# Kernel tuning notes

Hardware: AMD Instinct MI355X
Metric: run time of the kernel (lower is better)

## Reference

```python
import jax, jax.numpy as jnp
import numpy as np

FEATS = 768
HEAD = 12
HD = FEATS // HEAD


def setup_inputs() -> dict:
    key = jax.random.key(0)
    ks = jax.random.split(key, 10)
    b, n, f = 8, 1024, FEATS
    s = 1.0 / np.sqrt(f)
    return {
        "x": jax.random.normal(ks[0], (b, n, f), dtype=jnp.float32),
        "bias": jnp.zeros((), dtype=jnp.float32),
        "Wq": jax.random.normal(ks[1], (f, f), dtype=jnp.float32) * s,
        "bq": jnp.zeros((f,), dtype=jnp.float32),
        "Wk": jax.random.normal(ks[2], (f, f), dtype=jnp.float32) * s,
        "bk": jnp.zeros((f,), dtype=jnp.float32),
        "Wv": jax.random.normal(ks[3], (f, f), dtype=jnp.float32) * s,
        "bv": jnp.zeros((f,), dtype=jnp.float32),
        "Wo": jax.random.normal(ks[4], (f, f), dtype=jnp.float32) * s,
        "bo": jnp.zeros((f,), dtype=jnp.float32),
    }


def reference(x, bias, Wq, bq, Wk, bk, Wv, bv, Wo, bo):
    b, n, f = x.shape
    sqrt_d = jnp.sqrt(jnp.asarray(f, dtype=x.dtype))  # scale uses full feats, per source

    def split_heads(t):  # (b,n,f) -> (b,h,n,hd)
        return t.reshape(b, n, HEAD, HD).transpose(0, 2, 1, 3)

    q = split_heads(x @ Wq.T + bq)
    k = split_heads(x @ Wk.T + bk)
    v = split_heads(x @ Wv.T + bv)

    # sigmoid attention: no row-wise normalization
    score = jax.nn.sigmoid(jnp.einsum('bhif,bhjf->bhij', q, k) / sqrt_d + bias)
    attn = jnp.einsum('bhij,bhjf->bihf', score, v)  # (b,n,h,hd)
    o = attn.reshape(b, n, f) @ Wo.T + bo  # dropout p=0.0 -> identity
    return o
```

## Files before the change

### kernel.cpp

```cpp
#include <hip/hip_runtime.h>

#define FEATS 768
#define NHEAD 12
#define HD    64
#define SEQ   1024
#define NB    8
#define MROWS (NB*SEQ)
#define NQK   (2*FEATS)
#define QKVN  (3*FEATS)
#define QSC   0.0520616136f

typedef __attribute__((ext_vector_type(8))) __bf16          bf16x8;
typedef __attribute__((ext_vector_type(4))) __bf16          bf16x4;
typedef __attribute__((ext_vector_type(4))) unsigned short  us4;
typedef __attribute__((ext_vector_type(4))) float           f32x4;

__device__ __forceinline__ unsigned short f2bf(float f) {
  union { float f; unsigned u; } v; v.f = f;
  return (unsigned short)((v.u + 0x7fffu + ((v.u >> 16) & 1u)) >> 16);
}

__device__ __forceinline__ void gload_lds16(const void* g, void* l) {
  __builtin_amdgcn_global_load_lds(
      (const __attribute__((address_space(1))) void*)g,
      (__attribute__((address_space(3))) void*)l, 16, 0, 0);
}

__global__ void cast_all(const float* __restrict__ x,
                         const float* __restrict__ Wq, const float* __restrict__ Wk,
                         const float* __restrict__ Wv, const float* __restrict__ Wo,
                         const float* __restrict__ bq, const float* __restrict__ bk,
                         const float* __restrict__ bv,
                         unsigned short* __restrict__ Xbf,
                         unsigned short* __restrict__ Wcat,
                         unsigned short* __restrict__ Wobf,
                         float* __restrict__ bcat) {
  int blk = blockIdx.x;
  if (blk < 6144) {
    int i = blk * 256 + threadIdx.x;
    f32x4 v = ((const f32x4*)x)[i];
    us4 o;
    o[0] = f2bf(v[0]); o[1] = f2bf(v[1]); o[2] = f2bf(v[2]); o[3] = f2bf(v[3]);
    ((us4*)Xbf)[i] = o;
  } else if (blk < 8448) {
    int bb = blk - 6144;
    int mtx = bb / 576;
    int i = (bb % 576) * 256 + threadIdx.x;
    const float* src = (mtx == 0) ? Wq : (mtx == 1) ? Wk : (mtx == 2) ? Wv : Wo;
    f32x4 v = ((const f32x4*)src)[i];
    us4 o;
    o[0] = f2bf(v[0]); o[1] = f2bf(v[1]); o[2] = f2bf(v[2]); o[3] = f2bf(v[3]);
    if (mtx < 3) ((us4*)Wcat)[mtx * 147456 + i] = o;
    else         ((us4*)Wobf)[i] = o;
  } else {
    int i = (blk - 8448) * 256 + threadIdx.x;
    if (i < QKVN)
      bcat[i] = (i < FEATS) ? bq[i] : (i < 2*FEATS ? bk[i-FEATS] : bv[i-2*FEATS]);
  }
}

#define FOFF(row) ((row)*64 + (((g) ^ (((row) >> 1) & 3)) << 4))

__global__ __launch_bounds__(256, 3) void gemm1_bt(
    const unsigned short* __restrict__ A,
    const unsigned short* __restrict__ B,
    const float* __restrict__ bias,
    unsigned short* __restrict__ QKo,
    unsigned short* __restrict__ VTo)
{
  __shared__ __align__(16) char Al[2 * 8192];
  __shared__ __align__(16) char Bl[2 * 12288];

  const int tid  = threadIdx.x;
  const int lane = tid & 63;
  const int w    = tid >> 6;
  const int l15  = lane & 15;
  const int g    = lane >> 4;
  const int wm   = (w >> 1) * 64;
  const int wn   = (w & 1) * 96;

  const int id  = blockIdx.x;
  const int xcd = id & 7;
  const int j   = id >> 3;
  const int mi  = xcd * 8 + (j & 7);
  const int ni  = j >> 3;
  const int mbase = mi * 128;
  const int nbase = ni * 192;

  const int trow  = tid >> 2;
  const int sslot = ((tid & 3) ^ ((tid >> 3) & 3)) * 8;
  const unsigned short* Ag = A + (size_t)(mbase + trow) * 768 + sslot;
  const unsigned short* Bg = B + (size_t)(nbase + trow) * 768 + sslot;

  auto STAGE = [&](int buf, int t) {
    const unsigned short* sa = Ag + t * 32;
    const unsigned short* sb = Bg + t * 32;
    char* da = Al + buf * 8192  + tid * 16;
    char* db = Bl + buf * 12288 + tid * 16;
    gload_lds16(sa,            da);
    gload_lds16(sa + 64*768,   da + 4096);
    gload_lds16(sb,            db);
    gload_lds16(sb + 64*768,   db + 4096);
    gload_lds16(sb + 128*768,  db + 8192);
  };

  f32x4 acc[4][6] = {};

  STAGE(0, 0);
  asm volatile("s_waitcnt vmcnt(0)" ::: "memory");
  __builtin_amdgcn_s_barrier();

  for (int t = 0; t < 24; t++) {
    if (t < 23) STAGE((t + 1) & 1, t + 1);

    const char* Ab = Al + (t & 1) * 8192;
    const char* Bb = Bl + (t & 1) * 12288;
    bf16x8 af[4];
#pragma unroll
    for (int mf = 0; mf < 4; mf++) {
      const int row = wm + mf*16 + l15;
      af[mf] = *(const bf16x8*)(Ab + FOFF(row));
    }
    __builtin_amdgcn_s_setprio(1);
#pragma unroll
    for (int nf = 0; nf < 6; nf++) {
      const int row = wn + nf*16 + l15;
      bf16x8 bfv = *(const bf16x8*)(Bb + FOFF(row));
#pragma unroll
      for (int mf = 0; mf < 4; mf++)
        acc[mf][nf] = __builtin_amdgcn_mfma_f32_16x16x32_bf16(af[mf], bfv, acc[mf][nf], 0, 0, 0);
    }
    __builtin_amdgcn_s_setprio(0);

    if (t < 23) {
      asm volatile("s_waitcnt vmcnt(0)" ::: "memory");
      __builtin_amdgcn_s_barrier();
    }
  }

  const bool isQK = (ni < 8);
  const float osc = (ni < 4) ? QSC : 1.0f;
#pragma unroll
  for (int mf = 0; mf < 4; mf++)
#pragma unroll
    for (int nf = 0; nf < 6; nf++) {
      const int col  = nbase + wn + nf*16 + l15;
      const float bb = bias[col];
      const int row0 = mbase + wm + mf*16 + g*4;
      if (isQK) {
#pragma unroll
        for (int r = 0; r < 4; r++)
          QKo[(size_t)(row0 + r)*NQK + col] = f2bf((acc[mf][nf][r] + bb) * osc);
      } else {
        const int c  = col - NQK;
        const int hh = c >> 6, dd = c & 63;
        const int bI = row0 >> 10, n0 = row0 & 1023;
        us4 o;
#pragma unroll
        for (int r = 0; r < 4; r++) o[r] = f2bf(acc[mf][nf][r] + bb);
        *(us4*)(VTo + ((size_t)((bI*NHEAD + hh)*HD + dd))*SEQ + n0) = o;
      }
    }
}

__global__ __launch_bounds__(256, 4) void gemm2_bt(
    const unsigned short* __restrict__ A,
    const unsigned short* __restrict__ B,
    const float* __restrict__ bias,
    float* __restrict__ C)
{
  __shared__ __align__(16) char Al[2 * 4096];
  __shared__ __align__(16) char Bl[2 * 8192];

  const int tid  = threadIdx.x;
  const int lane = tid & 63;
  const int w    = tid >> 6;
  const int l15  = lane & 15;
  const int g    = lane >> 4;
  const int wm   = (w >> 1) * 32;
  const int wn   = (w & 1) * 64;

  const int id  = blockIdx.x;
  const int xcd = id & 7;
  const int j   = id >> 3;
  const int mi  = xcd * 16 + (j & 15);
  const int ni  = j >> 4;
  const int mbase = mi * 64;
  const int nbase = ni * 128;

  const int trow  = tid >> 2;
  const int sslot = ((tid & 3) ^ ((tid >> 3) & 3)) * 8;
  const unsigned short* Ag = A + (size_t)(mbase + trow) * 768 + sslot;
  const unsigned short* Bg = B + (size_t)(nbase + trow) * 768 + sslot;

  auto STAGE = [&](int buf, int t) {
    const unsigned short* sa = Ag + t * 32;
    const unsigned short* sb = Bg + t * 32;
    char* da = Al + buf * 4096 + tid * 16;
    char* db = Bl + buf * 8192 + tid * 16;
    gload_lds16(sa,           da);
    gload_lds16(sb,           db);
    gload_lds16(sb + 64*768,  db + 4096);
  };

  f32x4 acc[2][4] = {};

  STAGE(0, 0);
  asm volatile("s_waitcnt vmcnt(0)" ::: "memory");
  __builtin_amdgcn_s_barrier();

  for (int t = 0; t < 24; t++) {
    if (t < 23) STAGE((t + 1) & 1, t + 1);

    const char* Ab = Al + (t & 1) * 4096;
    const char* Bb = Bl + (t & 1) * 8192;
    bf16x8 af[2], bfv[4];
#pragma unroll
    for (int mf = 0; mf < 2; mf++) {
      const int row = wm + mf*16 + l15;
      af[mf] = *(const bf16x8*)(Ab + FOFF(row));
    }
#pragma unroll
    for (int nf = 0; nf < 4; nf++) {
      const int row = wn + nf*16 + l15;
      bfv[nf] = *(const bf16x8*)(Bb + FOFF(row));
    }
    __builtin_amdgcn_s_setprio(1);
#pragma unroll
    for (int mf = 0; mf < 2; mf++)
#pragma unroll
      for (int nf = 0; nf < 4; nf++)
        acc[mf][nf] = __builtin_amdgcn_mfma_f32_16x16x32_bf16(af[mf], bfv[nf], acc[mf][nf], 0, 0, 0);
    __builtin_amdgcn_s_setprio(0);

    if (t < 23) {
      asm volatile("s_waitcnt vmcnt(0)" ::: "memory");
      __builtin_amdgcn_s_barrier();
    }
  }

#pragma unroll
  for (int mf = 0; mf < 2; mf++)
#pragma unroll
    for (int nf = 0; nf < 4; nf++) {
      const int col  = nbase + wn + nf*16 + l15;
      const float bb = bias[col];
      const int row0 = mbase + wm + mf*16 + g*4;
#pragma unroll
      for (int r = 0; r < 4; r++)
        C[(size_t)(row0 + r)*FEATS + col] = acc[mf][nf][r] + bb;
    }
}
#undef FOFF

__global__ __launch_bounds__(256, 3) void attn_kernel(
    const unsigned short* __restrict__ QK,
    const unsigned short* __restrict__ VT,
    const float* __restrict__ biasp,
    unsigned short* __restrict__ AO)
{
  __shared__ __align__(16) char Kl[2][8192];
  __shared__ __align__(16) char Vl[2][8192];
  __shared__ __align__(16) char Sl[4][4096];

  const int tid  = threadIdx.x;
  const int lane = tid & 63;
  const int w    = tid >> 6;
  const int l15  = lane & 15;
  const int g    = lane >> 4;

  const int id  = blockIdx.x;
  const int r8  = id & 7;
  const int m   = id >> 3;
  const int bh  = r8 * 12 + (m >> 3);
  const int qx  = m & 7;
  const int b   = bh / NHEAD;
  const int h   = bh % NHEAD;
  const int rowB  = b * SEQ;
  const int qbase = rowB + qx * 128;

  const float Kb = __builtin_amdgcn_exp2f(-biasp[0] * 1.4426950408889634f);

  bf16x8 qf[2][2];
  {
    const unsigned short* qp = QK + (size_t)(qbase + w*32 + l15) * NQK + h*HD + g*8;
    qf[0][0] = *(const bf16x8*)(qp);
    qf[0][1] = *(const bf16x8*)(qp + 32);
    qf[1][0] = *(const bf16x8*)(qp + 16*NQK);
    qf[1][1] = *(const bf16x8*)(qp + 16*NQK + 32);
  }

  const int trow = tid >> 3;
  const int colb = ((tid & 7) * 16) ^ ((trow & 7) << 4);
  const char* Ksrc = (const char*)QK +
      ((size_t)(rowB + trow) * NQK + FEATS + h*HD) * 2 + colb;
  const char* Vsrc = (const char*)VT +
      ((size_t)(bh*HD + trow)) * (SEQ*2) + colb;

  auto STAGE_K = [&](int p, int t) {
    char* kw = Kl[p] + tid*16;
    gload_lds16(Ksrc + (size_t)t * 64 * (NQK*2),              kw);
    gload_lds16(Ksrc + (size_t)t * 64 * (NQK*2) + 32*(NQK*2), kw + 4096);
  };
  auto STAGE_V = [&](int p, int t) {
    char* vw = Vl[p] + tid*16;
    gload_lds16(Vsrc + t * 128,              vw);
    gload_lds16(Vsrc + t * 128 + 32*(SEQ*2), vw + 4096);
  };

  char* Sw = Sl[w];
  f32x4 o_acc[4][2] = {};
  f32x4 sE[2][4], sO[2][4];

  auto SIGPV = [&](f32x4 (&sP)[2][4], const char* Vp) {
#pragma unroll
    for (int qm = 0; qm < 2; qm++)
#pragma unroll
      for (int nf = 0; nf < 4; nf++) {
        bf16x4 pk;
#pragma unroll
        for (int rr = 0; rr < 4; rr++) {
          const float e = __builtin_amdgcn_exp2f(-sP[qm][nf][rr]);
          pk[rr] = (__bf16)__builtin_amdgcn_rcpf(__builtin_fmaf(Kb, e, 1.0f));
        }
        const int sq = qm*16 + l15;
        const int by = (sq*128 + (nf*16 + g*4)*2) ^ ((sq & 7) << 4);
        *(bf16x4*)(Sw + by) = pk;
      }
#pragma unroll
    for (int js = 0; js < 2; js++) {
      bf16x8 sf[2];
#pragma unroll
      for (int qm = 0; qm < 2; qm++) {
        const int sq = qm*16 + l15;
        const int by = (sq*128 + js*64 + g*16) ^ ((sq & 7) << 4);
        sf[qm] = *(const bf16x8*)(Sw + by);
      }
      bf16x8 vf[4];
#pragma unroll
      for (int df = 0; df < 4; df++) {
        const int row = df*16 + l15;
        const int by  = (row*128 + js*64 + g*16) ^ ((row & 7) << 4);
        vf[df] = *(const bf16x8*)(Vp + by);
      }
      __builtin_amdgcn_s_setprio(1);
#pragma unroll
      for (int df = 0; df < 4; df++)
#pragma unroll
        for (int qm = 0; qm < 2; qm++)
          o_acc[df][qm] = __builtin_amdgcn_mfma_f32_16x16x32_bf16(vf[df], sf[qm], o_acc[df][qm], 0, 0, 0);
      __builtin_amdgcn_s_setprio(0);
    }
  };

  auto BODY = [&](int t, f32x4 (&sC)[2][4], f32x4 (&sP)[2][4], bool stK, bool doPrev) {
    if (stK) STAGE_K((t + 1) & 1, t + 1);
    STAGE_V(t & 1, t);

    const char* Kp = Kl[t & 1];
#pragma unroll
    for (int qm = 0; qm < 2; qm++)
#pragma unroll
      for (int nf = 0; nf < 4; nf++)
        sC[qm][nf] = (f32x4){0.f, 0.f, 0.f, 0.f};
    __builtin_amdgcn_s_setprio(1);
#pragma unroll
    for (int nf = 0; nf < 4; nf++)
#pragma unroll
      for (int ks = 0; ks < 2; ks++) {
        const int row = nf*16 + l15;
        const int by  = (row*128 + ks*64 + g*16) ^ ((row & 7) << 4);
        bf16x8 kf = *(const bf16x8*)(Kp + by);
        sC[0][nf] = __builtin_amdgcn_mfma_f32_16x16x32_bf16(kf, qf[0][ks], sC[0][nf], 0, 0, 0);
        sC[1][nf] = __builtin_amdgcn_mfma_f32_16x16x32_bf16(kf, qf[1][ks], sC[1][nf], 0, 0, 0);
      }
    __builtin_amdgcn_s_setprio(0);

    if (doPrev) SIGPV(sP, Vl[(t - 1) & 1]);

    __syncthreads();
  };

  STAGE_K(0, 0);
  __syncthreads();

  BODY(0, sE, sO, true, false);
#pragma unroll 1
  for (int t = 1; t < 15; t += 2) {
    BODY(t,     sO, sE, true, true);
    BODY(t + 1, sE, sO, true, true);
  }
  BODY(15, sO, sE, false, true);
  SIGPV(sO, Vl[1]);

  unsigned short* aop = AO + (size_t)(qbase + w*32) * FEATS + h*HD;
#pragma unroll
  for (int df = 0; df < 4; df++)
#pragma unroll
    for (int qm = 0; qm < 2; qm++) {
      const int q  = qm*16 + l15;
      const int d0 = df*16 + g*4;
      bf16x4 o;
#pragma unroll
      for (int rr = 0; rr < 4; rr++) o[rr] = (__bf16)o_acc[df][qm][rr];
      *(bf16x4*)(aop + (size_t)q * FEATS + d0) = o;
    }
}

extern "C" void kernel_launch(void* const* d_in, const int* in_sizes, int n_in,
                              void* d_out, int out_size, void* d_ws, size_t ws_size,
                              hipStream_t stream) {
  const float* x    = (const float*)d_in[0];
  const float* bias = (const float*)d_in[1];
  const float* Wq   = (const float*)d_in[2];
  const float* bq   = (const float*)d_in[3];
  const float* Wk   = (const float*)d_in[4];
  const float* bk   = (const float*)d_in[5];
  const float* Wv   = (const float*)d_in[6];
  const float* bv   = (const float*)d_in[7];
  const float* Wo   = (const float*)d_in[8];
  const float* bo   = (const float*)d_in[9];
  float* out = (float*)d_out;

  char* ws = (char*)d_ws;
  unsigned short* Xbf  = (unsigned short*)(ws + 0);
  unsigned short* Wcat = (unsigned short*)(ws + 12582912);
  unsigned short* Wobf = (unsigned short*)(ws + 16121856);
  float*          bcat = (float*)        (ws + 17301504);
  unsigned short* QKb  = (unsigned short*)(ws + 17310720);
  unsigned short* VTb  = (unsigned short*)(ws + 42476544);
  unsigned short* AO   = Xbf;

  cast_all<<<8457, 256, 0, stream>>>(x, Wq, Wk, Wv, Wo, bq, bk, bv,
                                     Xbf, Wcat, Wobf, bcat);

  gemm1_bt<<<768, 256, 0, stream>>>(Xbf, Wcat, bcat, QKb, VTb);

  attn_kernel<<<768, 256, 0, stream>>>(QKb, VTb, bias, AO);

  gemm2_bt<<<768, 256, 0, stream>>>(AO, Wobf, bo, out);
}
```

Before: 108.1 us.

## Keep sigmoid scores in registers by permuting V^T key order

The QKV GEMM epilogue now writes V^T with a permuted key order inside each 64-key block, so the sigmoid scores produced by the QK^T MFMA can be fed directly as the B operand of the PV MFMA from registers. This removes the per-wave LDS scratch buffer and its write/read round trip, along with the associated LDS traffic and latency. LDS use per block drops, which may allow more resident blocks. The change relies on the producer and consumer agreeing exactly on the permutation.

```diff
diff --git a/kernel.cpp b/kernel.cpp
--- a/kernel.cpp
+++ b/kernel.cpp
@@ -155,10 +155,13 @@
         const int c  = col - NQK;
         const int hh = c >> 6, dd = c & 63;
         const int bI = row0 >> 10, n0 = row0 & 1023;
+        const int rl  = n0 & 63;
+        const int cp  = ((rl >> 5) << 5) | (((rl >> 2) & 3) << 3) | (((rl >> 4) & 1) << 2);
+        const int n0p = (n0 & ~63) | cp;
         us4 o;
 #pragma unroll
         for (int r = 0; r < 4; r++) o[r] = f2bf(acc[mf][nf][r] + bb);
-        *(us4*)(VTo + ((size_t)((bI*NHEAD + hh)*HD + dd))*SEQ + n0) = o;
+        *(us4*)(VTo + ((size_t)((bI*NHEAD + hh)*HD + dd))*SEQ + n0p) = o;
       }
     }
 }
@@ -261,7 +264,6 @@
 {
   __shared__ __align__(16) char Kl[2][8192];
   __shared__ __align__(16) char Vl[2][8192];
-  __shared__ __align__(16) char Sl[4][4096];
 
   const int tid  = threadIdx.x;
   const int lane = tid & 63;
@@ -308,34 +310,34 @@
     gload_lds16(Vsrc + t * 128 + 32*(SEQ*2), vw + 4096);
   };
 
-  char* Sw = Sl[w];
   f32x4 o_acc[4][2] = {};
   f32x4 sE[2][4], sO[2][4];
 
   auto SIGPV = [&](f32x4 (&sP)[2][4], const char* Vp) {
-#pragma unroll
-    for (int qm = 0; qm < 2; qm++)
-#pragma unroll
-      for (int nf = 0; nf < 4; nf++) {
-        bf16x4 pk;
+    bf16x8 paq[2][2];
+#pragma unroll
+    for (int qm = 0; qm < 2; qm++) {
+      float sg[4][4];
+#pragma unroll
+      for (int nf = 0; nf < 4; nf++)
 #pragma unroll
         for (int rr = 0; rr < 4; rr++) {
           const float e = __builtin_amdgcn_exp2f(-sP[qm][nf][rr]);
-          pk[rr] = (__bf16)__builtin_amdgcn_rcpf(__builtin_fmaf(Kb, e, 1.0f));
+          sg[nf][rr] = __builtin_amdgcn_rcpf(__builtin_fmaf(Kb, e, 1.0f));
         }
-        const int sq = qm*16 + l15;
-        const int by = (sq*128 + (nf*16 + g*4)*2) ^ ((sq & 7) << 4);
-        *(bf16x4*)(Sw + by) = pk;
+#pragma unroll
+      for (int js = 0; js < 2; js++) {
+        bf16x8 pa;
+#pragma unroll
+        for (int jj = 0; jj < 4; jj++) {
+          pa[jj]     = (__bf16)sg[2*js][jj];
+          pa[jj + 4] = (__bf16)sg[2*js + 1][jj];
+        }
+        paq[qm][js] = pa;
       }
+    }
 #pragma unroll
     for (int js = 0; js < 2; js++) {
-      bf16x8 sf[2];
-#pragma unroll
-      for (int qm = 0; qm < 2; qm++) {
-        const int sq = qm*16 + l15;
-        const int by = (sq*128 + js*64 + g*16) ^ ((sq & 7) << 4);
-        sf[qm] = *(const bf16x8*)(Sw + by);
-      }
       bf16x8 vf[4];
 #pragma unroll
       for (int df = 0; df < 4; df++) {
@@ -348,7 +350,7 @@
       for (int df = 0; df < 4; df++)
 #pragma unroll
         for (int qm = 0; qm < 2; qm++)
-          o_acc[df][qm] = __builtin_amdgcn_mfma_f32_16x16x32_bf16(vf[df], sf[qm], o_acc[df][qm], 0, 0, 0);
+          o_acc[df][qm] = __builtin_amdgcn_mfma_f32_16x16x32_bf16(vf[df], paq[qm][js], o_acc[df][qm], 0, 0, 0);
       __builtin_amdgcn_s_setprio(0);
     }
   };
```

Result: faster. 106.0 us (-2.0%).
